# Kernel optimization log

Measured on AMD Instinct MI355X. Metric: run time of the kernel, lower is better.

Reference implementation:

```python
import jax, jax.numpy as jnp
import numpy as np

D_MODEL, STATE, N_EXP, VOCAB = 1024, 16, 4, 32000
B, L = 4, 2048
EPS = 1e-5


def setup_inputs() -> dict:
    key = jax.random.key(0)
    ks = jax.random.split(key, 20)
    d, s, e, f = D_MODEL, STATE, N_EXP, 4 * D_MODEL
    sc = 0.02
    inp = {
        "x": jax.random.normal(ks[0], (B, L, d), jnp.float32),
        "A_log": jnp.log(jax.random.uniform(ks[1], (d, s)) * 0.9 + 0.1),
        "D_param": jnp.ones((d,), jnp.float32),
        "Wd": jax.random.normal(ks[2], (d, d)) * sc,
        "bd": jnp.zeros((d,)),
        "WB": jax.random.normal(ks[3], (d, s)) * sc,
        "bB": jnp.zeros((s,)),
        "WC": jax.random.normal(ks[4], (d, s)) * sc,
        "bC": jnp.zeros((s,)),
        "Wr": jax.random.normal(ks[5], (d, e)) * sc,
        "br": jnp.zeros((e,)),
        "up_w": jax.random.normal(ks[6], (e, d, f)) * sc,
        "up_b": jnp.zeros((e, f)),
        "down_w": jax.random.normal(ks[7], (e, f, d)) * sc,
        "down_b": jnp.zeros((e, d)),
        "ln_w": jnp.ones((d,)),
        "ln_b": jnp.zeros((d,)),
    }
    return inp


def reference(x, A_log, D_param, Wd, bd, WB, bB, WC, bC, Wr, br,
              up_w, up_b, down_w, down_b, ln_w, ln_b):
    Bb, Ll, d = x.shape
    delta = jax.nn.softplus(jnp.einsum('bld,de->ble', x, Wd) + bd)   # [B,L,D]
    Bm = jnp.einsum('bld,ds->bls', x, WB) + bB                        # [B,L,S]
    Cm = jnp.einsum('bld,ds->bls', x, WC) + bC                        # [B,L,S]
    A = -jnp.exp(A_log)                                               # [D,S]

    def step(h, inps):
        x_t, d_t, B_t, C_t = inps                                     # [B,D],[B,D],[B,S],[B,S]
        bar_A = jnp.exp(jnp.minimum(d_t[:, :, None] * A, 2.0))        # [B,D,S]
        bar_B = jnp.clip(d_t[:, :, None] * B_t[:, None, :], -2.0, 2.0)
        h = jnp.clip(bar_A * h + bar_B * x_t[:, :, None], -100.0, 100.0)
        y = jnp.sum(h * C_t[:, None, :], axis=-1) + x_t * D_param     # [B,D]
        return h, y

    h0 = jnp.zeros((Bb, d, STATE), x.dtype)
    xs = (jnp.swapaxes(x, 0, 1), jnp.swapaxes(delta, 0, 1),
          jnp.swapaxes(Bm, 0, 1), jnp.swapaxes(Cm, 0, 1))
    _, ys = jax.lax.scan(step, h0, xs)                                # ys: [L,B,D]
    ssm_out = jnp.swapaxes(ys, 0, 1)                                  # [B,L,D]

    flat = ssm_out.reshape(-1, d)                                     # [N,D]
    routing = jax.nn.softmax(flat @ Wr + br, axis=1)                  # [N,E]
    top1_w = jnp.max(routing, axis=1)                                 # [N]
    top1_i = jnp.argmax(routing, axis=1)                              # [N]

    hid = jax.nn.silu(jnp.einsum('nd,edf->enf', flat, up_w) + up_b[:, None, :])
    all_out = jnp.einsum('enf,efd->end', hid, down_w) + down_b[:, None, :]  # [E,N,D]
    sel = jnp.take_along_axis(jnp.swapaxes(all_out, 0, 1),
                              top1_i[:, None, None], axis=1)[:, 0, :]  # [N,D]
    moe_out = (sel * top1_w[:, None]).reshape(Bb, Ll, d)

    out = ssm_out + moe_out
    mu = jnp.mean(out, axis=-1, keepdims=True)
    var = jnp.mean((out - mu) ** 2, axis=-1, keepdims=True)
    return (out - mu) * jax.lax.rsqrt(var + EPS) * ln_w + ln_b
```

## Files before the change

kernel.cpp:

```cpp
#include <hip/hip_runtime.h>

typedef __attribute__((ext_vector_type(4))) float f32x4;
typedef __attribute__((ext_vector_type(8))) short short8;
typedef __attribute__((ext_vector_type(8))) unsigned short ushort8;
typedef __attribute__((ext_vector_type(4))) unsigned short ushort4v;

#define DEV __device__ __forceinline__

constexpr int NTOK = 8192;
constexpr int NCP  = 1152;
constexpr int MAXTILES = 68;
constexpr int NPAD = MAXTILES * 128;
constexpr int NCHUNK = 16;
constexpr int CLEN = 2048 / NCHUNK;

DEV unsigned short f2bf(float f) {
  unsigned int u = __builtin_bit_cast(unsigned int, f);
  u += 0x7FFFu + ((u >> 16) & 1u);
  return (unsigned short)(u >> 16);
}
DEV float bf2f(unsigned short h) {
  unsigned int u = ((unsigned int)h) << 16;
  return __builtin_bit_cast(float, u);
}

DEV int swz(int e) { return e ^ (((e >> 6) & 7) << 3); }

__global__ __launch_bounds__(256) void conv_x_k(const float* __restrict__ x,
    unsigned short* __restrict__ xh, unsigned short* __restrict__ xl) {
  int i = (blockIdx.x * 256 + threadIdx.x) * 4;
  f32x4 v = *(const f32x4*)(x + i);
  ushort4v hv, lv;
#pragma unroll
  for (int j = 0; j < 4; ++j) {
    unsigned short hh = f2bf(v[j]);
    hv[j] = hh;
    lv[j] = f2bf(v[j] - bf2f(hh));
  }
  *(ushort4v*)(xh + i) = hv;
  *(ushort4v*)(xl + i) = lv;
}

__global__ __launch_bounds__(256) void conv_w_k(const float* __restrict__ Wd,
    const float* __restrict__ WB, const float* __restrict__ WC,
    unsigned short* __restrict__ wh, unsigned short* __restrict__ wl) {
  int o = blockIdx.x * 256 + threadIdx.x;
  int k = o & 1023, n = o >> 10;
  float v = 0.f;
  if (n < 1024) v = Wd[k * 1024 + n];
  else if (n < 1040) v = WB[k * 16 + (n - 1024)];
  else if (n < 1056) v = WC[k * 16 + (n - 1040)];
  unsigned short hh = f2bf(v);
  wh[o] = hh;
  wl[o] = f2bf(v - bf2f(hh));
}

__global__ __launch_bounds__(256) void trans_k(const float* __restrict__ in,
    unsigned short* __restrict__ out, int R, int C) {
  __shared__ float tile[32][33];
  int e = blockIdx.z;
  int r0 = blockIdx.y * 32, c0 = blockIdx.x * 32;
  int r = threadIdx.x >> 5, cc = threadIdx.x & 31;
  const float* src = in + ((size_t)e * R + r0) * C + c0;
#pragma unroll
  for (int j = 0; j < 4; ++j) tile[r + j * 8][cc] = src[(size_t)(r + j * 8) * C + cc];
  __syncthreads();
  unsigned short* dst = out + ((size_t)e * C + c0) * R + r0;
#pragma unroll
  for (int j = 0; j < 4; ++j) dst[(size_t)(r + j * 8) * R + cc] = f2bf(tile[cc][r + j * 8]);
}

template<int MODE>
__global__ __launch_bounds__(256) void gemm_k(
    const unsigned short* __restrict__ A, const unsigned short* __restrict__ A2,
    const unsigned short* __restrict__ Bm, const unsigned short* __restrict__ B2,
    float* __restrict__ outF, float* __restrict__ outF2, unsigned short* __restrict__ outH,
    const float* __restrict__ bias, const float* __restrict__ b1, const float* __restrict__ b2,
    const int* __restrict__ perm, const float* __restrict__ t1w,
    const int* __restrict__ tile_e, const int* __restrict__ tile_r0,
    const int* __restrict__ tile_ve, const int* __restrict__ n_tiles)
{
  constexpr bool SPLIT = (MODE == 0);
  constexpr int KT  = (MODE == 2) ? 32 : 16;
  constexpr int NT  = (MODE == 0) ? 64 : 68;
  __shared__ __align__(16) unsigned short lA[(SPLIT ? 2 : 1) * 128 * 64];
  __shared__ __align__(16) unsigned short lB[(SPLIT ? 2 : 1) * 128 * 64];

  const int t = threadIdx.x;
  int lin = blockIdx.x + NT * blockIdx.y;
  int x = lin & 7, tt = lin >> 3;
  int rowtile, colblk, kz = 0;
  if constexpr (MODE == 0) {
    colblk = tt >> 3; rowtile = x * 8 + (tt & 7);
  } else if constexpr (MODE == 1) {
    int cnt = (x < 4) ? 9 : 8;
    int r0 = x * 8 + (x < 4 ? x : 4);
    if (tt < cnt * 32) { colblk = tt / cnt; rowtile = r0 + tt % cnt; }
    else {
      int sp = (x - 4) * 16 + (tt - 256);
      int ox = sp >> 4, ot = 272 + (sp & 15);
      colblk = ot / 9; rowtile = ox * 9 + ot % 9;
    }
  } else {
    int pr;
    if (tt < 128) { int g = tt >> 6, r6 = tt & 63; colblk = r6 >> 3; pr = g * 8 + (r6 & 7); }
    else { colblk = tt - 128; pr = 16; }
    int pair = x * 17 + pr;
    kz = pair / 68; rowtile = pair % 68;
  }

  int e = 0, row0 = 0, vend = 0;
  if constexpr (MODE == 0) {
    row0 = rowtile * 128;
  } else {
    if (rowtile >= *n_tiles) return;
    e = tile_e[rowtile]; row0 = tile_r0[rowtile]; vend = tile_ve[rowtile];
  }
  (void)vend;

  const int r8 = t >> 3;
  const int kc = (t & 7) * 8;
  const unsigned short* ap[4];
  const unsigned short* bp[4];
  ptrdiff_t da = 0, db = 0;
  if constexpr (SPLIT) { da = A2 - A; db = B2 - Bm; }
#pragma unroll
  for (int j = 0; j < 4; ++j) {
    int r = row0 + r8 + 32 * j;
    if constexpr (MODE == 1) {
      int tok = perm[r];
      ap[j] = A + (size_t)tok * 1024 + kc;
    } else if constexpr (MODE == 2) {
      ap[j] = A + (size_t)r * 4096 + kz * 2048 + kc;
    } else {
      ap[j] = A + (size_t)r * 1024 + kc;
    }
    int cb = colblk * 128 + r8 + 32 * j;
    if constexpr (MODE == 0) bp[j] = Bm + (size_t)cb * 1024 + kc;
    else if constexpr (MODE == 1) bp[j] = Bm + ((size_t)e * 4096 + cb) * 1024 + kc;
    else bp[j] = Bm + ((size_t)e * 1024 + cb) * 4096 + kz * 2048 + kc;
  }

  const int w = t >> 6, lane = t & 63;
  const int wm = w >> 1, wn = w & 1;
  const int lr = lane & 15, lk = (lane >> 4) * 8;
  int wOf[4];
  int aoffs[4][2], boffs[4][2];
#pragma unroll
  for (int j = 0; j < 4; ++j) wOf[j] = swz(j * 2048 + t * 8);
#pragma unroll
  for (int i = 0; i < 4; ++i) {
    int ae = (wm * 64 + i * 16 + lr) * 64 + lk;
    int be = (wn * 64 + i * 16 + lr) * 64 + lk;
#pragma unroll
    for (int kk = 0; kk < 2; ++kk) {
      aoffs[i][kk] = swz(ae + kk * 32);
      boffs[i][kk] = swz(be + kk * 32);
    }
  }

  f32x4 acc[4][4];
#pragma unroll
  for (int i = 0; i < 4; ++i)
#pragma unroll
    for (int j = 0; j < 4; ++j) acc[i][j] = (f32x4)(0.f);

  ushort8 va[4], vb[4], va2[4], vb2[4];
#pragma unroll
  for (int j = 0; j < 4; ++j) {
    va[j] = *(const ushort8*)(ap[j]);
    vb[j] = *(const ushort8*)(bp[j]);
    if constexpr (SPLIT) {
      va2[j] = *(const ushort8*)(ap[j] + da);
      vb2[j] = *(const ushort8*)(bp[j] + db);
    }
    ap[j] += 64; bp[j] += 64;
  }

  for (int kt = 0; kt < KT; ++kt) {
    __syncthreads();
    {
#pragma unroll
      for (int j = 0; j < 4; ++j) {
        *(ushort8*)(lA + wOf[j]) = va[j];
        *(ushort8*)(lB + wOf[j]) = vb[j];
        if constexpr (SPLIT) {
          *(ushort8*)(lA + 8192 + wOf[j]) = va2[j];
          *(ushort8*)(lB + 8192 + wOf[j]) = vb2[j];
        }
      }
    }
    if (kt + 1 < KT) {
#pragma unroll
      for (int j = 0; j < 4; ++j) {
        va[j] = *(const ushort8*)(ap[j]);
        vb[j] = *(const ushort8*)(bp[j]);
        if constexpr (SPLIT) {
          va2[j] = *(const ushort8*)(ap[j] + da);
          vb2[j] = *(const ushort8*)(bp[j] + db);
        }
        ap[j] += 64; bp[j] += 64;
      }
    }
    __syncthreads();
#pragma unroll
    for (int kk = 0; kk < 2; ++kk) {
      short8 af[4], bfv[4], afl[4], bfl[4];
#pragma unroll
      for (int i = 0; i < 4; ++i) {
        af[i]  = *(const short8*)(lA + aoffs[i][kk]);
        bfv[i] = *(const short8*)(lB + boffs[i][kk]);
        if constexpr (SPLIT) {
          afl[i] = *(const short8*)(lA + 8192 + aoffs[i][kk]);
          bfl[i] = *(const short8*)(lB + 8192 + boffs[i][kk]);
        }
      }
#pragma unroll
      for (int mi = 0; mi < 4; ++mi)
#pragma unroll
        for (int ni = 0; ni < 4; ++ni) {
          acc[mi][ni] = __builtin_amdgcn_mfma_f32_16x16x32_bf16(af[mi], bfv[ni], acc[mi][ni], 0, 0, 0);
          if constexpr (SPLIT) {
            acc[mi][ni] = __builtin_amdgcn_mfma_f32_16x16x32_bf16(afl[mi], bfv[ni], acc[mi][ni], 0, 0, 0);
            acc[mi][ni] = __builtin_amdgcn_mfma_f32_16x16x32_bf16(af[mi], bfl[ni], acc[mi][ni], 0, 0, 0);
          }
        }
    }
  }

#pragma unroll
  for (int mi = 0; mi < 4; ++mi) {
#pragma unroll
    for (int ni = 0; ni < 4; ++ni) {
      int col = colblk * 128 + wn * 64 + ni * 16 + lr;
#pragma unroll
      for (int q = 0; q < 4; ++q) {
        int rl = wm * 64 + mi * 16 + (lane >> 4) * 4 + q;
        float v = acc[mi][ni][q];
        if constexpr (MODE == 0) {
          if (col < 1056) {
            float v2;
            if (col < 1024) {
              float z = v + bias[col];
              v2 = fmaxf(z, 0.f) + __logf(1.f + __expf(-fabsf(z)));
            } else if (col < 1040) {
              v2 = v + b1[col - 1024];
            } else {
              v2 = v + b2[col - 1040];
            }
            outF[(size_t)(row0 + rl) * NCP + col] = v2;
          }
        } else if constexpr (MODE == 1) {
          float z = v + bias[e * 4096 + col];
          float sg = 1.f / (1.f + __expf(-z));
          outH[(size_t)(row0 + rl) * 4096 + col] = f2bf(z * sg);
        } else {
          int pos = row0 + rl;
          if (pos < vend) {
            int tok = perm[pos];
            float bb_ = kz ? bias[e * 1024 + col] : 0.f;
            float val = (v + bb_) * t1w[tok];
            float* dst = kz ? outF2 : outF;
            dst[(size_t)tok * 1024 + col] = val;
          }
        }
      }
    }
  }
}

constexpr int SPF = 4;

template<int PASS>
__global__ __launch_bounds__(256) void scan_p(
    const float* __restrict__ P, const float* __restrict__ x,
    const float* __restrict__ A_log, const float* __restrict__ D_param,
    float* __restrict__ Ap, float* __restrict__ He, const float* __restrict__ Hi,
    float* __restrict__ ssm, unsigned short* __restrict__ ssmbf)
{
  const int t = threadIdx.x;
  const int s = t & 15, dlane = t >> 4;
  const int blk = blockIdx.x;
  const int c  = blk & 15;
  const int dg = (blk >> 4) & 63;
  const int b  = blk >> 10;
  const int d  = dg * 16 + dlane;
  const float Ads = -__expf(A_log[d * 16 + s]);
  const float Dp = D_param[d];
  const float* Pb = P + ((size_t)b * 2048 + (size_t)c * CLEN) * NCP;
  const float* xb = x + ((size_t)b * 2048 + (size_t)c * CLEN) * 1024;
  const size_t sidx = (size_t)c * 65536 + ((size_t)b * 1024 + d) * 16 + s;

  float h = (PASS == 1) ? 0.f : Hi[sidx];
  float ap = 1.f;

  float dl0[SPF], br0[SPF], cr0[SPF], xr0[SPF];
  auto LOADB = [&](int base, float* dd, float* bb, float* cc2, float* xx) {
#pragma unroll
    for (int j = 0; j < SPF; ++j) {
      const float* Pt = Pb + (size_t)(base + j) * NCP;
      dd[j] = Pt[d];
      bb[j] = Pt[1024 + s];
      if constexpr (PASS == 3) cc2[j] = Pt[1040 + s];
      xx[j] = xb[(size_t)(base + j) * 1024 + d];
    }
  };
  LOADB(0, dl0, br0, cr0, xr0);
  size_t obase = ((size_t)b * 2048 + (size_t)c * CLEN) * 1024 + d;
  constexpr int NBAT = CLEN / SPF;
  for (int bb = 0; bb < NBAT; ++bb) {
    float dl1[SPF], br1[SPF], cr1[SPF], xr1[SPF];
    if (bb + 1 < NBAT) LOADB((bb + 1) * SPF, dl1, br1, cr1, xr1);
#pragma unroll
    for (int j = 0; j < SPF; ++j) {
      float delta = dl0[j];
      float barA = __expf(delta * Ads);
      float barB = fminf(fmaxf(delta * br0[j], -2.f), 2.f);
      h = fminf(fmaxf(barA * h + barB * xr0[j], -100.f), 100.f);
      if constexpr (PASS == 1) {
        ap *= barA;
      } else {
        float y = h * cr0[j];
        y += __shfl_xor(y, 1); y += __shfl_xor(y, 2);
        y += __shfl_xor(y, 4); y += __shfl_xor(y, 8);
        if (s == 0) {
          float val = y + xr0[j] * Dp;
          size_t o = obase + (size_t)(bb * SPF + j) * 1024;
          ssm[o] = val;
          ssmbf[o] = f2bf(val);
        }
      }
    }
    if (bb + 1 < NBAT) {
#pragma unroll
      for (int j = 0; j < SPF; ++j) { dl0[j]=dl1[j]; br0[j]=br1[j]; cr0[j]=cr1[j]; xr0[j]=xr1[j]; }
    }
  }
  if constexpr (PASS == 1) {
    Ap[sidx] = ap;
    He[sidx] = h;
  }
}

__global__ __launch_bounds__(256) void scan_c(const float* __restrict__ Ap,
    const float* __restrict__ He, float* __restrict__ Hi)
{
  int i = blockIdx.x * 256 + threadIdx.x;
  float h = 0.f;
#pragma unroll
  for (int c = 0; c < NCHUNK; ++c) {
    size_t idx = (size_t)c * 65536 + i;
    Hi[idx] = h;
    h = Ap[idx] * h + He[idx];
  }
}

__global__ __launch_bounds__(256) void route_k(
    const float* __restrict__ ssm, const float* __restrict__ Wr, const float* __restrict__ br,
    float* __restrict__ t1w, int* __restrict__ t1i, int* __restrict__ counts)
{
  int w = threadIdx.x >> 6, lane = threadIdx.x & 63;
  int n = blockIdx.x * 4 + w;
  const float* row = ssm + (size_t)n * 1024;
  float a0 = 0, a1 = 0, a2 = 0, a3 = 0;
  for (int i = lane; i < 1024; i += 64) {
    float v = row[i];
    f32x4 wr = *(const f32x4*)(Wr + i * 4);
    a0 += v * wr[0]; a1 += v * wr[1]; a2 += v * wr[2]; a3 += v * wr[3];
  }
#pragma unroll
  for (int off = 32; off; off >>= 1) {
    a0 += __shfl_xor(a0, off); a1 += __shfl_xor(a1, off);
    a2 += __shfl_xor(a2, off); a3 += __shfl_xor(a3, off);
  }
  a0 += br[0]; a1 += br[1]; a2 += br[2]; a3 += br[3];
  float m = a0; int idx = 0;
  if (a1 > m) { m = a1; idx = 1; }
  if (a2 > m) { m = a2; idx = 2; }
  if (a3 > m) { m = a3; idx = 3; }
  float denom = __expf(a0 - m) + __expf(a1 - m) + __expf(a2 - m) + __expf(a3 - m);
  if (lane == 0) {
    t1w[n] = 1.f / denom;
    t1i[n] = idx;
    atomicAdd(&counts[idx], 1);
  }
}

__global__ void build_k(int* misc, int* perm)
{
  if (threadIdx.x != 0 || blockIdx.x != 0) return;
  int* counts = misc; int* cursors = misc + 4; int* base = misc + 8;
  int* ntiles = misc + 12; int* te = misc + 16; int* tr = misc + 96; int* tv = misc + 176;
  int bpos = 0, tt = 0;
  for (int e = 0; e < 4; ++e) {
    base[e] = bpos; cursors[e] = 0;
    int c = counts[e];
    int nt = (c + 127) >> 7;
    for (int i = 0; i < nt; ++i) { te[tt] = e; tr[tt] = bpos + i * 128; tv[tt] = bpos + c; ++tt; }
    for (int p = bpos + c; p < bpos + nt * 128; ++p) perm[p] = 0;
    bpos += nt * 128;
  }
  *ntiles = tt;
}

__global__ __launch_bounds__(256) void scatter_k(const int* __restrict__ t1i,
    int* misc, int* __restrict__ perm)
{
  int n = blockIdx.x * 256 + threadIdx.x;
  int e = t1i[n];
  int pos = atomicAdd(&misc[4 + e], 1);
  perm[misc[8 + e] + pos] = n;
}

__global__ __launch_bounds__(256) void ln_k(
    float* __restrict__ out, const float* __restrict__ ssm,
    const float* __restrict__ P0, const float* __restrict__ P1,
    const float* __restrict__ lnw, const float* __restrict__ lnb)
{
  __shared__ float red[8];
  int n = blockIdx.x, t = threadIdx.x;
  size_t base = (size_t)n * 1024 + t * 4;
  f32x4 p0 = *(const f32x4*)(P0 + base);
  f32x4 p1 = *(const f32x4*)(P1 + base);
  f32x4 bsm = *(const f32x4*)(ssm + base);
  float o[4]; float sum = 0, sq = 0;
#pragma unroll
  for (int j = 0; j < 4; ++j) { o[j] = p0[j] + p1[j] + bsm[j]; sum += o[j]; sq += o[j] * o[j]; }
#pragma unroll
  for (int off = 32; off; off >>= 1) { sum += __shfl_xor(sum, off); sq += __shfl_xor(sq, off); }
  int w = t >> 6;
  if ((t & 63) == 0) { red[w] = sum; red[4 + w] = sq; }
  __syncthreads();
  sum = red[0] + red[1] + red[2] + red[3];
  sq  = red[4] + red[5] + red[6] + red[7];
  float mu = sum * (1.f / 1024.f);
  float var = sq * (1.f / 1024.f) - mu * mu;
  float rs = rsqrtf(var + 1e-5f);
  f32x4 r;
#pragma unroll
  for (int j = 0; j < 4; ++j) {
    int c = t * 4 + j;
    r[j] = (o[j] - mu) * rs * lnw[c] + lnb[c];
  }
  *(f32x4*)(out + base) = r;
}

extern "C" void kernel_launch(void* const* d_in, const int* in_sizes, int n_in,
                              void* d_out, int out_size, void* d_ws, size_t ws_size,
                              hipStream_t stream)
{
  (void)in_sizes; (void)n_in; (void)out_size;
  const float* x       = (const float*)d_in[0];
  const float* A_log   = (const float*)d_in[1];
  const float* D_param = (const float*)d_in[2];
  const float* Wd      = (const float*)d_in[3];
  const float* bd      = (const float*)d_in[4];
  const float* WB      = (const float*)d_in[5];
  const float* bB      = (const float*)d_in[6];
  const float* WC      = (const float*)d_in[7];
  const float* bC      = (const float*)d_in[8];
  const float* Wr      = (const float*)d_in[9];
  const float* br      = (const float*)d_in[10];
  const float* up_w    = (const float*)d_in[11];
  const float* up_b    = (const float*)d_in[12];
  const float* down_w  = (const float*)d_in[13];
  const float* down_b  = (const float*)d_in[14];
  const float* ln_w    = (const float*)d_in[15];
  const float* ln_b    = (const float*)d_in[16];
  float* out = (float*)d_out;

  char* ws = (char*)d_ws;
  size_t off = 0;
  auto alloc = [&](size_t bytes) { size_t o = off; off += (bytes + 255) & ~(size_t)255; return o; };
  size_t oXh  = alloc((size_t)NTOK * 1024 * 2);
  size_t oXl  = alloc((size_t)NTOK * 1024 * 2);
  size_t oWh  = alloc((size_t)NCP * 1024 * 2);
  size_t oWl  = alloc((size_t)NCP * 1024 * 2);
  size_t oP   = alloc((size_t)NTOK * NCP * 4);
  size_t oSSM = alloc((size_t)NTOK * 1024 * 4);
  size_t oSBF = alloc((size_t)NTOK * 1024 * 2);
  size_t oUp  = alloc((size_t)4 * 4096 * 1024 * 2);
  size_t oDn  = alloc((size_t)4 * 4096 * 1024 * 2);
  size_t oHid = alloc((size_t)NPAD * 4096 * 2);
  size_t oT1w = alloc((size_t)NTOK * 4);
  size_t oT1i = alloc((size_t)NTOK * 4);
  size_t oPerm= alloc((size_t)NPAD * 4);
  size_t oMisc= alloc(1024);
  if (ws_size < off) return;

  unsigned short* Xh  = (unsigned short*)(ws + oXh);
  unsigned short* Xl  = (unsigned short*)(ws + oXl);
  unsigned short* Wh  = (unsigned short*)(ws + oWh);
  unsigned short* Wl  = (unsigned short*)(ws + oWl);
  float*          Pf  = (float*)(ws + oP);
  float*          SSM = (float*)(ws + oSSM);
  unsigned short* SBF = (unsigned short*)(ws + oSBF);
  unsigned short* UpT = (unsigned short*)(ws + oUp);
  unsigned short* DnT = (unsigned short*)(ws + oDn);
  unsigned short* Hid = (unsigned short*)(ws + oHid);
  float*          T1w = (float*)(ws + oT1w);
  int*            T1i = (int*)(ws + oT1i);
  int*            perm= (int*)(ws + oPerm);
  int*            misc= (int*)(ws + oMisc);
  float*          ApB = (float*)(ws + oHid);
  float*          HeB = ApB + (size_t)NCHUNK * 65536;
  float*          HiB = HeB + (size_t)NCHUNK * 65536;
  float*          Pk0 = (float*)(ws + oP);
  float*          Pk1 = (float*)(ws + oXh);

  hipMemsetAsync(misc, 0, 16, stream);
  conv_x_k <<<8192, 256, 0, stream>>>(x, Xh, Xl);
  conv_w_k <<<4608, 256, 0, stream>>>(Wd, WB, WC, Wh, Wl);
  trans_k<<<dim3(128, 32, 4), 256, 0, stream>>>(up_w, UpT, 1024, 4096);
  trans_k<<<dim3(32, 128, 4), 256, 0, stream>>>(down_w, DnT, 4096, 1024);

  gemm_k<0><<<dim3(64, 9), 256, 0, stream>>>(Xh, Xl, Wh, Wl, Pf, nullptr, nullptr,
      bd, bB, bC, nullptr, nullptr, nullptr, nullptr, nullptr, nullptr);

  scan_p<1><<<4096, 256, 0, stream>>>(Pf, x, A_log, D_param, ApB, HeB, nullptr, nullptr, nullptr);
  scan_c   <<<256, 256, 0, stream>>>(ApB, HeB, HiB);
  scan_p<3><<<4096, 256, 0, stream>>>(Pf, x, A_log, D_param, nullptr, nullptr, HiB, SSM, SBF);

  route_k<<<2048, 256, 0, stream>>>(SSM, Wr, br, T1w, T1i, misc);
  build_k<<<1, 1, 0, stream>>>(misc, perm);
  scatter_k<<<32, 256, 0, stream>>>(T1i, misc, perm);

  gemm_k<1><<<dim3(68, 32), 256, 0, stream>>>(SBF, nullptr, UpT, nullptr,
      nullptr, nullptr, Hid, up_b, nullptr, nullptr, perm, nullptr,
      misc + 16, misc + 96, misc + 176, misc + 12);
  gemm_k<2><<<dim3(68, 16), 256, 0, stream>>>(Hid, nullptr, DnT, nullptr,
      Pk0, Pk1, nullptr, down_b, nullptr, nullptr, perm, T1w,
      misc + 16, misc + 96, misc + 176, misc + 12);

  ln_k<<<8192, 256, 0, stream>>>(out, SSM, Pk0, Pk1, ln_w, ln_b);
}
```

Measured before the change: 801.6 us.

## Double-buffer LDS tiles with register prefetch in non-split GEMM modes

For the MODE 1/2 GEMMs (the MoE up/down projections), shared-memory A/B tiles are now double-buffered, with two sets of prefetch registers. One barrier per k-step replaces two, and the next tile is written to the alternate LDS buffer while the current one feeds the MFMAs. The aim is to overlap global loads and LDS writes with matrix compute and to cut synchronization stalls. In exchange, LDS per block doubles for these modes and register pressure rises, which may reduce occupancy.

```diff
diff --git a/kernel.cpp b/kernel.cpp
--- a/kernel.cpp
+++ b/kernel.cpp
@@ -83,8 +83,8 @@
   constexpr bool SPLIT = (MODE == 0);
   constexpr int KT  = (MODE == 2) ? 32 : 16;
   constexpr int NT  = (MODE == 0) ? 64 : 68;
-  __shared__ __align__(16) unsigned short lA[(SPLIT ? 2 : 1) * 128 * 64];
-  __shared__ __align__(16) unsigned short lB[(SPLIT ? 2 : 1) * 128 * 64];
+  __shared__ __align__(16) unsigned short lA[2 * 128 * 64];
+  __shared__ __align__(16) unsigned short lB[2 * 128 * 64];
 
   const int t = threadIdx.x;
   int lin = blockIdx.x + NT * blockIdx.y;
@@ -165,66 +165,108 @@
 #pragma unroll
     for (int j = 0; j < 4; ++j) acc[i][j] = (f32x4)(0.f);
 
-  ushort8 va[4], vb[4], va2[4], vb2[4];
-#pragma unroll
-  for (int j = 0; j < 4; ++j) {
-    va[j] = *(const ushort8*)(ap[j]);
-    vb[j] = *(const ushort8*)(bp[j]);
-    if constexpr (SPLIT) {
+  if constexpr (SPLIT) {
+    ushort8 va[4], vb[4], va2[4], vb2[4];
+#pragma unroll
+    for (int j = 0; j < 4; ++j) {
+      va[j] = *(const ushort8*)(ap[j]);
+      vb[j] = *(const ushort8*)(bp[j]);
       va2[j] = *(const ushort8*)(ap[j] + da);
       vb2[j] = *(const ushort8*)(bp[j] + db);
-    }
-    ap[j] += 64; bp[j] += 64;
-  }
-
-  for (int kt = 0; kt < KT; ++kt) {
-    __syncthreads();
-    {
+      ap[j] += 64; bp[j] += 64;
+    }
+    for (int kt = 0; kt < KT; ++kt) {
+      __syncthreads();
 #pragma unroll
       for (int j = 0; j < 4; ++j) {
         *(ushort8*)(lA + wOf[j]) = va[j];
         *(ushort8*)(lB + wOf[j]) = vb[j];
-        if constexpr (SPLIT) {
-          *(ushort8*)(lA + 8192 + wOf[j]) = va2[j];
-          *(ushort8*)(lB + 8192 + wOf[j]) = vb2[j];
-        }
-      }
-    }
-    if (kt + 1 < KT) {
-#pragma unroll
-      for (int j = 0; j < 4; ++j) {
-        va[j] = *(const ushort8*)(ap[j]);
-        vb[j] = *(const ushort8*)(bp[j]);
-        if constexpr (SPLIT) {
+        *(ushort8*)(lA + 8192 + wOf[j]) = va2[j];
+        *(ushort8*)(lB + 8192 + wOf[j]) = vb2[j];
+      }
+      if (kt + 1 < KT) {
+#pragma unroll
+        for (int j = 0; j < 4; ++j) {
+          va[j] = *(const ushort8*)(ap[j]);
+          vb[j] = *(const ushort8*)(bp[j]);
           va2[j] = *(const ushort8*)(ap[j] + da);
           vb2[j] = *(const ushort8*)(bp[j] + db);
+          ap[j] += 64; bp[j] += 64;
         }
-        ap[j] += 64; bp[j] += 64;
-      }
-    }
-    __syncthreads();
-#pragma unroll
-    for (int kk = 0; kk < 2; ++kk) {
-      short8 af[4], bfv[4], afl[4], bfl[4];
-#pragma unroll
-      for (int i = 0; i < 4; ++i) {
-        af[i]  = *(const short8*)(lA + aoffs[i][kk]);
-        bfv[i] = *(const short8*)(lB + boffs[i][kk]);
-        if constexpr (SPLIT) {
+      }
+      __syncthreads();
+#pragma unroll
+      for (int kk = 0; kk < 2; ++kk) {
+        short8 af[4], bfv[4], afl[4], bfl[4];
+#pragma unroll
+        for (int i = 0; i < 4; ++i) {
+          af[i]  = *(const short8*)(lA + aoffs[i][kk]);
+          bfv[i] = *(const short8*)(lB + boffs[i][kk]);
           afl[i] = *(const short8*)(lA + 8192 + aoffs[i][kk]);
           bfl[i] = *(const short8*)(lB + 8192 + boffs[i][kk]);
         }
-      }
-#pragma unroll
-      for (int mi = 0; mi < 4; ++mi)
-#pragma unroll
-        for (int ni = 0; ni < 4; ++ni) {
-          acc[mi][ni] = __builtin_amdgcn_mfma_f32_16x16x32_bf16(af[mi], bfv[ni], acc[mi][ni], 0, 0, 0);
-          if constexpr (SPLIT) {
+#pragma unroll
+        for (int mi = 0; mi < 4; ++mi)
+#pragma unroll
+          for (int ni = 0; ni < 4; ++ni) {
+            acc[mi][ni] = __builtin_amdgcn_mfma_f32_16x16x32_bf16(af[mi], bfv[ni], acc[mi][ni], 0, 0, 0);
             acc[mi][ni] = __builtin_amdgcn_mfma_f32_16x16x32_bf16(afl[mi], bfv[ni], acc[mi][ni], 0, 0, 0);
             acc[mi][ni] = __builtin_amdgcn_mfma_f32_16x16x32_bf16(af[mi], bfl[ni], acc[mi][ni], 0, 0, 0);
           }
+      }
+    }
+  } else {
+    ushort8 pAa[4], pAb[4], pBa[4], pBb[4];
+    auto LOADR = [&](ushort8* ra, ushort8* rb, int kt) {
+#pragma unroll
+      for (int j = 0; j < 4; ++j) {
+        ra[j] = *(const ushort8*)(ap[j] + (size_t)kt * 64);
+        rb[j] = *(const ushort8*)(bp[j] + (size_t)kt * 64);
+      }
+    };
+    auto WRITE = [&](int buf, ushort8* ra, ushort8* rb) {
+      unsigned short* la = lA + buf * 8192;
+      unsigned short* lb = lB + buf * 8192;
+#pragma unroll
+      for (int j = 0; j < 4; ++j) {
+        *(ushort8*)(la + wOf[j]) = ra[j];
+        *(ushort8*)(lb + wOf[j]) = rb[j];
+      }
+    };
+    auto COMPUTE = [&](int buf) {
+      const unsigned short* la = lA + buf * 8192;
+      const unsigned short* lb = lB + buf * 8192;
+#pragma unroll
+      for (int kk = 0; kk < 2; ++kk) {
+        short8 af[4], bfv[4];
+#pragma unroll
+        for (int i = 0; i < 4; ++i) {
+          af[i]  = *(const short8*)(la + aoffs[i][kk]);
+          bfv[i] = *(const short8*)(lb + boffs[i][kk]);
         }
+#pragma unroll
+        for (int mi = 0; mi < 4; ++mi)
+#pragma unroll
+          for (int ni = 0; ni < 4; ++ni)
+            acc[mi][ni] = __builtin_amdgcn_mfma_f32_16x16x32_bf16(af[mi], bfv[ni], acc[mi][ni], 0, 0, 0);
+      }
+    };
+
+    LOADR(pAa, pAb, 0);
+    WRITE(0, pAa, pAb);
+    LOADR(pAa, pAb, 1);
+    int cur = 0;
+    for (int kt = 0; kt < KT; kt += 2) {
+      __syncthreads();
+      if (kt + 2 < KT) LOADR(pBa, pBb, kt + 2);
+      if (kt + 1 < KT) WRITE(cur ^ 1, pAa, pAb);
+      COMPUTE(cur);
+      cur ^= 1;
+      __syncthreads();
+      if (kt + 3 < KT) LOADR(pAa, pAb, kt + 3);
+      if (kt + 2 < KT) WRITE(cur ^ 1, pBa, pBb);
+      COMPUTE(cur);
+      cur ^= 1;
     }
   }
 
```

Result: slower. 952.9 us (+18.9%).
